# Performance work log

Hardware: AMD Instinct MI355X
Metric: run time of the kernel (lower is better)

## Reference

```python
import jax, jax.numpy as jnp
import numpy as np

N = 50000      # nodes (cells)
E = 800000     # directed edges
IN, H1, H2, Z = 512, 128, 128, 64


def setup_inputs() -> dict:
    key = jax.random.key(0)
    ks = jax.random.split(key, 12)
    x = jax.random.normal(ks[0], (N, IN), jnp.float32)
    edge_index = jax.random.randint(ks[1], (2, E), 0, N, dtype=jnp.int64)

    def glorot(k, i, o):
        return jax.random.normal(k, (i, o), jnp.float32) * np.float32(1.0 / np.sqrt(i))

    return {
        "x": x,
        "edge_index": edge_index,
        "W1": glorot(ks[2], IN, H1), "b1": jnp.zeros((H1,), jnp.float32),
        "W2": glorot(ks[3], H1, H2), "b2": jnp.zeros((H2,), jnp.float32),
        "Wm": glorot(ks[4], H2, Z),  "bm": jnp.zeros((Z,), jnp.float32),
        "Ws": glorot(ks[5], H2, Z),  "bs": jnp.zeros((Z,), jnp.float32),
    }


def _gcn_norm(edge_index, n):
    # PyG GCNConv default: add self-loops, sym-normalize D^-1/2 (A+I) D^-1/2
    loops = jnp.arange(n, dtype=edge_index.dtype)
    src = jnp.concatenate([edge_index[0], loops])
    dst = jnp.concatenate([edge_index[1], loops])
    deg = jax.ops.segment_sum(jnp.ones_like(dst, jnp.float32), dst, num_segments=n)
    dis = jnp.where(deg > 0, jax.lax.rsqrt(jnp.maximum(deg, 1.0)), 0.0)
    norm = dis[src] * dis[dst]  # [E+N]
    return src, dst, norm


def _gcn_conv(x, W, b, src, dst, norm, n):
    h = x @ W                          # [N, out] transform first
    msg = h[src] * norm[:, None]       # gather + scale
    out = jax.ops.segment_sum(msg, dst, num_segments=n)  # scatter-add at targets
    return out + b


def reference(x, edge_index, W1, b1, W2, b2, Wm, bm, Ws, bs):
    n = x.shape[0]
    src, dst, norm = _gcn_norm(edge_index, n)
    h = jax.nn.relu(_gcn_conv(x, W1, b1, src, dst, norm, n))
    h = jax.nn.relu(_gcn_conv(h, W2, b2, src, dst, norm, n))
    # dropout p=0.4 is identity in eval mode
    z_mean = _gcn_conv(h, Wm, bm, src, dst, norm, n)
    z_log_std = _gcn_conv(h, Ws, bs, src, dst, norm, n)
    return (z_mean, z_log_std)
```

## Files before the change

### kernel.cpp

```cpp
#include <hip/hip_runtime.h>


using u16 = unsigned short;
typedef __attribute__((ext_vector_type(8))) short short8;
typedef __attribute__((ext_vector_type(4))) float f32x4;

__device__ __forceinline__ void split_bf16(float f, u16& hi, u16& lo) {
    unsigned b = __float_as_uint(f);
    hi = (u16)(b >> 16);
    float rem = f - __uint_as_float(b & 0xFFFF0000u);
    lo = (u16)(__float_as_uint(rem) >> 16);
}

__device__ __forceinline__ int block_mode(const int* __restrict__ ew, int* sflag) {
    if (threadIdx.x == 0) *sflag = 0;
    __syncthreads();
    if (ew[2 * (int)threadIdx.x + 1] != 0) atomicOr(sflag, 1);
    __syncthreads();
    return *sflag ? 0 : 1;
}

__global__ void deg_kernel(const int* __restrict__ ew, int* __restrict__ deg, int E) {
    __shared__ int sflag;
    int mode = block_mode(ew, &sflag);
    int e = blockIdx.x * blockDim.x + threadIdx.x;
    if (e >= E) return;
    int d = mode ? ew[2 * E + 2 * e] : ew[E + e];
    atomicAdd(&deg[d], 1);
}

__global__ void scan_block_kernel(const int* __restrict__ deg, int* __restrict__ rowptr,
                                  int* __restrict__ aux, float* __restrict__ dis, int N) {
    __shared__ int s[256];
    int i = blockIdx.x * 256 + threadIdx.x;
    int v = (i < N) ? deg[i] : 0;
    if (i < N) dis[i] = rsqrtf((float)v + 1.0f);
    s[threadIdx.x] = v;
    __syncthreads();
    for (int off = 1; off < 256; off <<= 1) {
        int t = (threadIdx.x >= off) ? s[threadIdx.x - off] : 0;
        __syncthreads();
        s[threadIdx.x] += t;
        __syncthreads();
    }
    if (i < N) rowptr[i] = s[threadIdx.x] - v;
    if (threadIdx.x == 255) aux[blockIdx.x] = s[255];
}

__global__ void scan_aux_kernel(int* __restrict__ aux, int nb) {
    __shared__ int s[256];
    int i = threadIdx.x;
    int v = (i < nb) ? aux[i] : 0;
    s[i] = v;
    __syncthreads();
    for (int off = 1; off < 256; off <<= 1) {
        int t = (i >= off) ? s[i - off] : 0;
        __syncthreads();
        s[i] += t;
        __syncthreads();
    }
    if (i < nb) aux[i] = s[i] - v;
}

__global__ void add_offsets_kernel(int* __restrict__ rowptr, const int* __restrict__ aux,
                                   int N, int E) {
    int i = blockIdx.x * 256 + threadIdx.x;
    if (i < N) rowptr[i] += aux[i >> 8];
    if (i == 0) rowptr[N] = E;
}

__global__ void fill_csr_kernel(const int* __restrict__ ew,
                                const int* __restrict__ rowptr, int* __restrict__ cursor,
                                int* __restrict__ csr_src, int E) {
    __shared__ int sflag;
    int mode = block_mode(ew, &sflag);
    int e = blockIdx.x * blockDim.x + threadIdx.x;
    if (e >= E) return;
    int s = mode ? ew[2 * e] : ew[e];
    int d = mode ? ew[2 * E + 2 * e] : ew[E + e];
    int pos = rowptr[d] + atomicAdd(&cursor[d], 1);
    csr_src[pos] = s;
}

__global__ void conv_all_kernel(const float* __restrict__ W1, const float* __restrict__ W2,
                                const float* __restrict__ Wm, const float* __restrict__ Ws,
                                u16* __restrict__ W1t_hi, u16* __restrict__ W1t_lo,
                                u16* __restrict__ W2t_hi, u16* __restrict__ W2t_lo,
                                u16* __restrict__ Wct_hi, u16* __restrict__ Wct_lo) {
    int idx = blockIdx.x * 256 + threadIdx.x;
    u16 h, l;
    if (idx < 65536) {
        int k = idx >> 7, n = idx & 127;
        split_bf16(W1[idx], h, l);
        W1t_hi[n * 512 + k] = h;
        W1t_lo[n * 512 + k] = l;
    } else if (idx < 81920) {
        int t = idx - 65536;
        int k = t >> 7, n = t & 127;
        split_bf16(W2[t], h, l);
        W2t_hi[n * 128 + k] = h;
        W2t_lo[n * 128 + k] = l;
    } else if (idx < 98304) {
        int t = idx - 81920;
        int k = t >> 7, j = t & 127;
        float f = (j < 64) ? Wm[k * 64 + j] : Ws[k * 64 + (j - 64)];
        split_bf16(f, h, l);
        Wct_hi[j * 128 + k] = h;
        Wct_lo[j * 128 + k] = l;
    }
}

__global__ __launch_bounds__(256) void gemm_mfma(const float* __restrict__ A,
                                                 const u16* __restrict__ Bt_hi,
                                                 const u16* __restrict__ Bt_lo,
                                                 float* __restrict__ C,
                                                 int N, int K) {
    const int tid = threadIdx.x;
    const int w = tid >> 6, lane = tid & 63;
    const int m16 = lane & 15, quad = lane >> 4;

    const int nrt = (N + 31) >> 5;
    const int wtile = blockIdx.x * 4 + w;
    if (wtile >= 2 * nrt) return;
    const int rt = wtile >> 1;
    const int c0 = (wtile & 1) << 6;
    const int row0 = rt << 5;

    int r0 = row0 + m16;      if (r0 > N - 1) r0 = N - 1;
    int r1 = row0 + 16 + m16; if (r1 > N - 1) r1 = N - 1;
    const float* ap0 = A + (size_t)r0 * K + quad * 8;
    const float* ap1 = A + (size_t)r1 * K + quad * 8;
    const u16* bph = Bt_hi + (size_t)(c0 + m16) * K + quad * 8;
    const u16* bpl = Bt_lo + (size_t)(c0 + m16) * K + quad * 8;
    const size_t bstr = (size_t)16 * K;

    f32x4 acc[2][4];
#pragma unroll
    for (int i = 0; i < 2; ++i)
#pragma unroll
        for (int j = 0; j < 4; ++j) acc[i][j] = (f32x4)0.f;

    f32x4 x0, x1, x2, x3;
    f32x4 y0, y1, y2, y3;

    auto lda = [&](f32x4& v0, f32x4& v1, f32x4& v2, f32x4& v3, int kk) {
        const float* p0 = ap0 + kk * 32;
        const float* p1 = ap1 + kk * 32;
        v0 = *(const f32x4*)p0;
        v1 = *(const f32x4*)(p0 + 4);
        v2 = *(const f32x4*)p1;
        v3 = *(const f32x4*)(p1 + 4);
    };
    auto cvt = [&](const f32x4& v0, const f32x4& v1, short8& h, short8& l) {
#pragma unroll
        for (int q = 0; q < 4; ++q) {
            u16 hh, ll;
            split_bf16(v0[q], hh, ll);
            h[q] = (short)hh;
            l[q] = (short)ll;
            split_bf16(v1[q], hh, ll);
            h[4 + q] = (short)hh;
            l[4 + q] = (short)ll;
        }
    };
    auto step = [&](f32x4& v0, f32x4& v1, f32x4& v2, f32x4& v3,
                    int kk, int kpre, bool pre) {
        short8 bh[4], bl[4];
#pragma unroll
        for (int j = 0; j < 4; ++j) {
            bh[j] = *(const short8*)(bph + bstr * j + kk * 32);
            bl[j] = *(const short8*)(bpl + bstr * j + kk * 32);
        }
        short8 ah[2], al[2];
        cvt(v0, v1, ah[0], al[0]);
        cvt(v2, v3, ah[1], al[1]);
        if (pre) lda(v0, v1, v2, v3, kpre);
#pragma unroll
        for (int i = 0; i < 2; ++i)
#pragma unroll
            for (int j = 0; j < 4; ++j) {
                acc[i][j] = __builtin_amdgcn_mfma_f32_16x16x32_bf16(
                    ah[i], bh[j], acc[i][j], 0, 0, 0);
                acc[i][j] = __builtin_amdgcn_mfma_f32_16x16x32_bf16(
                    ah[i], bl[j], acc[i][j], 0, 0, 0);
                acc[i][j] = __builtin_amdgcn_mfma_f32_16x16x32_bf16(
                    al[i], bh[j], acc[i][j], 0, 0, 0);
            }
    };

    const int ksteps = K >> 5;
    lda(x0, x1, x2, x3, 0);
    lda(y0, y1, y2, y3, 1);
    int ks = 0;
    for (; ks + 2 < ksteps; ks += 2) {
        step(x0, x1, x2, x3, ks, ks + 2, true);
        step(y0, y1, y2, y3, ks + 1, ks + 3, true);
    }
    step(x0, x1, x2, x3, ks, 0, false);
    step(y0, y1, y2, y3, ks + 1, 0, false);

#pragma unroll
    for (int i = 0; i < 2; ++i) {
#pragma unroll
        for (int r = 0; r < 4; ++r) {
            int gr = row0 + i * 16 + quad * 4 + r;
            if (gr < N) {
#pragma unroll
                for (int j = 0; j < 4; ++j)
                    C[(size_t)gr * 128 + c0 + j * 16 + m16] = acc[i][j][r];
            }
        }
    }
}

__global__ __launch_bounds__(256) void propagate_kernel(
    const float* __restrict__ h, const int* __restrict__ rowptr,
    const int* __restrict__ csr_src, const float* __restrict__ dis,
    const float* __restrict__ bias, float* __restrict__ out, int N, int do_relu) {
    int wave = (blockIdx.x * 256 + threadIdx.x) >> 6;
    int lane = threadIdx.x & 63;
    if (wave >= N) return;
    int v = wave;
    int f = lane * 2;
    float dv = dis[v];
    float ax = 0.f, ay = 0.f;
    int beg = rowptr[v], end = rowptr[v + 1];
    int i = beg;
    for (; i + 8 <= end; i += 8) {
        int s[8];
        float ww[8];
        float2 g[8];
#pragma unroll
        for (int u = 0; u < 8; ++u) s[u] = csr_src[i + u];
#pragma unroll
        for (int u = 0; u < 8; ++u) ww[u] = dis[s[u]];
#pragma unroll
        for (int u = 0; u < 8; ++u) g[u] = *(const float2*)&h[(size_t)s[u] * 128 + f];
#pragma unroll
        for (int u = 0; u < 8; ++u) {
            float t = ww[u] * dv;
            ax += t * g[u].x;
            ay += t * g[u].y;
        }
    }
    if (i + 4 <= end) {
        int s[4];
        float ww[4];
        float2 g[4];
#pragma unroll
        for (int u = 0; u < 4; ++u) s[u] = csr_src[i + u];
#pragma unroll
        for (int u = 0; u < 4; ++u) ww[u] = dis[s[u]];
#pragma unroll
        for (int u = 0; u < 4; ++u) g[u] = *(const float2*)&h[(size_t)s[u] * 128 + f];
#pragma unroll
        for (int u = 0; u < 4; ++u) {
            float t = ww[u] * dv;
            ax += t * g[u].x;
            ay += t * g[u].y;
        }
        i += 4;
    }
    for (; i < end; ++i) {
        int s = csr_src[i];
        float ws = dis[s] * dv;
        float2 g = *(const float2*)&h[(size_t)s * 128 + f];
        ax += ws * g.x;
        ay += ws * g.y;
    }
    float2 hv = *(const float2*)&h[(size_t)v * 128 + f];
    ax += dv * dv * hv.x;
    ay += dv * dv * hv.y;
    ax += bias[f];
    ay += bias[f + 1];
    if (do_relu) { ax = fmaxf(ax, 0.f); ay = fmaxf(ay, 0.f); }
    *(float2*)&out[(size_t)v * 128 + f] = make_float2(ax, ay);
}

__global__ __launch_bounds__(256) void propagate_final_kernel(
    const float* __restrict__ h, const int* __restrict__ rowptr,
    const int* __restrict__ csr_src, const float* __restrict__ dis,
    const float* __restrict__ bm, const float* __restrict__ bs,
    float* __restrict__ out, int N) {
    int wave = (blockIdx.x * 256 + threadIdx.x) >> 6;
    int lane = threadIdx.x & 63;
    if (wave >= N) return;
    int v = wave;
    int f = lane * 2;
    float dv = dis[v];
    float ax = 0.f, ay = 0.f;
    int beg = rowptr[v], end = rowptr[v + 1];
    int i = beg;
    for (; i + 8 <= end; i += 8) {
        int s[8];
        float ww[8];
        float2 g[8];
#pragma unroll
        for (int u = 0; u < 8; ++u) s[u] = csr_src[i + u];
#pragma unroll
        for (int u = 0; u < 8; ++u) ww[u] = dis[s[u]];
#pragma unroll
        for (int u = 0; u < 8; ++u) g[u] = *(const float2*)&h[(size_t)s[u] * 128 + f];
#pragma unroll
        for (int u = 0; u < 8; ++u) {
            float t = ww[u] * dv;
            ax += t * g[u].x;
            ay += t * g[u].y;
        }
    }
    if (i + 4 <= end) {
        int s[4];
        float ww[4];
        float2 g[4];
#pragma unroll
        for (int u = 0; u < 4; ++u) s[u] = csr_src[i + u];
#pragma unroll
        for (int u = 0; u < 4; ++u) ww[u] = dis[s[u]];
#pragma unroll
        for (int u = 0; u < 4; ++u) g[u] = *(const float2*)&h[(size_t)s[u] * 128 + f];
#pragma unroll
        for (int u = 0; u < 4; ++u) {
            float t = ww[u] * dv;
            ax += t * g[u].x;
            ay += t * g[u].y;
        }
        i += 4;
    }
    for (; i < end; ++i) {
        int s = csr_src[i];
        float ws = dis[s] * dv;
        float2 g = *(const float2*)&h[(size_t)s * 128 + f];
        ax += ws * g.x;
        ay += ws * g.y;
    }
    float2 hv = *(const float2*)&h[(size_t)v * 128 + f];
    ax += dv * dv * hv.x;
    ay += dv * dv * hv.y;
    if (f < 64) {
        *(float2*)&out[(size_t)v * 64 + f] = make_float2(ax + bm[f], ay + bm[f + 1]);
    } else {
        int g = f - 64;
        *(float2*)&out[(size_t)N * 64 + (size_t)v * 64 + g] =
            make_float2(ax + bs[g], ay + bs[g + 1]);
    }
}

extern "C" void kernel_launch(void* const* d_in, const int* in_sizes, int n_in,
                              void* d_out, int out_size, void* d_ws, size_t ws_size,
                              hipStream_t stream) {
    const float* x  = (const float*)d_in[0];
    const int*   ew = (const int*)d_in[1];
    const float* W1 = (const float*)d_in[2];
    const float* b1 = (const float*)d_in[3];
    const float* W2 = (const float*)d_in[4];
    const float* b2 = (const float*)d_in[5];
    const float* Wm = (const float*)d_in[6];
    const float* bm = (const float*)d_in[7];
    const float* Ws = (const float*)d_in[8];
    const float* bs = (const float*)d_in[9];
    float* out = (float*)d_out;

    const int IN = 512, H = 128;
    const int N = in_sizes[0] / IN;
    const int E = in_sizes[1] / 2;

    char* base = (char*)d_ws;
    size_t off = 0;
    auto alloc = [&](size_t bytes) -> char* {
        char* p = base + off;
        off = (off + bytes + 255) & ~(size_t)255;
        return p;
    };
    char*  degcur  = (char*) alloc(400384);
    float* dis     = (float*)alloc((size_t)N * 4);
    int*   rowptr  = (int*)  alloc((size_t)(N + 1) * 4);
    int*   aux     = (int*)  alloc(256 * 4);
    int*   csr_src = (int*)  alloc((size_t)E * 4);
    u16*   W1t_hi  = (u16*)  alloc((size_t)IN * H * 2);
    u16*   W1t_lo  = (u16*)  alloc((size_t)IN * H * 2);
    u16*   W2t_hi  = (u16*)  alloc((size_t)H * H * 2);
    u16*   W2t_lo  = (u16*)  alloc((size_t)H * H * 2);
    u16*   Wct_hi  = (u16*)  alloc((size_t)H * H * 2);
    u16*   Wct_lo  = (u16*)  alloc((size_t)H * H * 2);
    float* hA      = (float*)alloc((size_t)N * H * 4);
    float* hB      = (float*)alloc((size_t)N * H * 4);
    (void)ws_size; (void)n_in; (void)out_size;

    int* deg    = (int*)degcur;
    int* cursor = (int*)(degcur + 200192);

    hipMemsetAsync(degcur, 0, 400384, stream);

    const int eblocks = (E + 255) / 256;
    const int nblocks = (N + 255) / 256;

    conv_all_kernel<<<(98304 + 255) / 256, 256, 0, stream>>>(
        W1, W2, Wm, Ws, W1t_hi, W1t_lo, W2t_hi, W2t_lo, Wct_hi, Wct_lo);
    deg_kernel<<<eblocks, 256, 0, stream>>>(ew, deg, E);
    scan_block_kernel<<<nblocks, 256, 0, stream>>>(deg, rowptr, aux, dis, N);
    scan_aux_kernel<<<1, 256, 0, stream>>>(aux, nblocks);
    add_offsets_kernel<<<nblocks, 256, 0, stream>>>(rowptr, aux, N, E);
    fill_csr_kernel<<<eblocks, 256, 0, stream>>>(ew, rowptr, cursor, csr_src, E);

    const int wtiles = 2 * ((N + 31) / 32);
    const int gblocks = (wtiles + 3) / 4;
    const int pblocks = (N * 64 + 255) / 256;

    gemm_mfma<<<gblocks, 256, 0, stream>>>(x, W1t_hi, W1t_lo, hA, N, IN);
    propagate_kernel<<<pblocks, 256, 0, stream>>>(hA, rowptr, csr_src, dis,
                                                  b1, hB, N, 1);
    gemm_mfma<<<gblocks, 256, 0, stream>>>(hB, W2t_hi, W2t_lo, hA, N, H);
    propagate_kernel<<<pblocks, 256, 0, stream>>>(hA, rowptr, csr_src, dis,
                                                  b2, hB, N, 1);
    gemm_mfma<<<gblocks, 256, 0, stream>>>(hB, Wct_hi, Wct_lo, hA, N, H);
    propagate_final_kernel<<<pblocks, 256, 0, stream>>>(hA, rowptr, csr_src, dis,
                                                        bm, bs, out, N);
}
```

Before: 551.3 us.

## Stage GEMM B tiles in double-buffered shared memory shared across waves

The GEMM block now covers a 64x128 output tile, with four waves that share the B (weight) fragments staged cooperatively through double-buffered LDS, padded to avoid bank conflicts. Previously each wave loaded its B fragments directly from global memory. The change is meant to cut redundant global and L2 traffic for the weights. In exchange it adds a __syncthreads per K step and LDS pressure. Since the weights are small and already cache-resident, the gain may be limited, and the whole pipeline is dominated by the propagate kernels.

```diff
diff --git a/kernel.cpp b/kernel.cpp
--- a/kernel.cpp
+++ b/kernel.cpp
@@ -110,29 +110,36 @@
     }
 }
 
+#define TILE_OFF(t) ((t) * 520)
+
 __global__ __launch_bounds__(256) void gemm_mfma(const float* __restrict__ A,
                                                  const u16* __restrict__ Bt_hi,
                                                  const u16* __restrict__ Bt_lo,
                                                  float* __restrict__ C,
                                                  int N, int K) {
+    __shared__ __align__(16) u16 BsH[2][8 * 520], BsL[2][8 * 520];
+
     const int tid = threadIdx.x;
     const int w = tid >> 6, lane = tid & 63;
     const int m16 = lane & 15, quad = lane >> 4;
 
-    const int nrt = (N + 31) >> 5;
-    const int wtile = blockIdx.x * 4 + w;
-    if (wtile >= 2 * nrt) return;
-    const int rt = wtile >> 1;
-    const int c0 = (wtile & 1) << 6;
-    const int row0 = rt << 5;
-
-    int r0 = row0 + m16;      if (r0 > N - 1) r0 = N - 1;
-    int r1 = row0 + 16 + m16; if (r1 > N - 1) r1 = N - 1;
+    const int row0 = blockIdx.x * 64;
+    const int R = (w >> 1) * 32;
+    const int c0 = (w & 1) << 6;
+    const int btile = (w & 1) * 4;
+
+    const int s_bc = tid >> 1;
+    const int s_bk = (tid & 1) * 16;
+    const int b_q0 = (tid & 1) * 2;
+    const int b_dst0 = TILE_OFF(s_bc >> 4) + ((s_bc & 15) + 16 * (b_q0 + 0)) * 8;
+    const int b_dst1 = TILE_OFF(s_bc >> 4) + ((s_bc & 15) + 16 * (b_q0 + 1)) * 8;
+    const u16* bph = Bt_hi + (size_t)s_bc * K + s_bk;
+    const u16* bpl = Bt_lo + (size_t)s_bc * K + s_bk;
+
+    int r0 = row0 + R + m16;      if (r0 > N - 1) r0 = N - 1;
+    int r1 = row0 + R + 16 + m16; if (r1 > N - 1) r1 = N - 1;
     const float* ap0 = A + (size_t)r0 * K + quad * 8;
     const float* ap1 = A + (size_t)r1 * K + quad * 8;
-    const u16* bph = Bt_hi + (size_t)(c0 + m16) * K + quad * 8;
-    const u16* bpl = Bt_lo + (size_t)(c0 + m16) * K + quad * 8;
-    const size_t bstr = (size_t)16 * K;
 
     f32x4 acc[2][4];
 #pragma unroll
@@ -142,7 +149,20 @@
 
     f32x4 x0, x1, x2, x3;
     f32x4 y0, y1, y2, y3;
-
+    short8 rbh0, rbh1, rbl0, rbl1;
+
+    auto ldb = [&](int kk) {
+        rbh0 = *(const short8*)(bph + kk * 32);
+        rbh1 = *(const short8*)(bph + kk * 32 + 8);
+        rbl0 = *(const short8*)(bpl + kk * 32);
+        rbl1 = *(const short8*)(bpl + kk * 32 + 8);
+    };
+    auto stb = [&](int buf) {
+        *(short8*)&BsH[buf][b_dst0] = rbh0;
+        *(short8*)&BsH[buf][b_dst1] = rbh1;
+        *(short8*)&BsL[buf][b_dst0] = rbl0;
+        *(short8*)&BsL[buf][b_dst1] = rbl1;
+    };
     auto lda = [&](f32x4& v0, f32x4& v1, f32x4& v2, f32x4& v3, int kk) {
         const float* p0 = ap0 + kk * 32;
         const float* p1 = ap1 + kk * 32;
@@ -163,47 +183,56 @@
             l[4 + q] = (short)ll;
         }
     };
-    auto step = [&](f32x4& v0, f32x4& v1, f32x4& v2, f32x4& v3,
-                    int kk, int kpre, bool pre) {
-        short8 bh[4], bl[4];
+
+    const int ksteps = K >> 5;
+    ldb(0);
+    lda(x0, x1, x2, x3, 0);
+    lda(y0, y1, y2, y3, 1);
+    stb(0);
+    ldb(1);
+
+    for (int ks = 0; ks < ksteps; ++ks) {
+        const int buf = ks & 1;
+        __syncthreads();
+        if (ks + 1 < ksteps) stb(buf ^ 1);
+        if (ks + 2 < ksteps) ldb(ks + 2);
+
+        short8 fbh[4], fbl[4];
 #pragma unroll
         for (int j = 0; j < 4; ++j) {
-            bh[j] = *(const short8*)(bph + bstr * j + kk * 32);
-            bl[j] = *(const short8*)(bpl + bstr * j + kk * 32);
-        }
+            fbh[j] = *(const short8*)&BsH[buf][TILE_OFF(btile + j) + lane * 8];
+            fbl[j] = *(const short8*)&BsL[buf][TILE_OFF(btile + j) + lane * 8];
+        }
+
         short8 ah[2], al[2];
-        cvt(v0, v1, ah[0], al[0]);
-        cvt(v2, v3, ah[1], al[1]);
-        if (pre) lda(v0, v1, v2, v3, kpre);
+        if (buf) {
+            cvt(y0, y1, ah[0], al[0]);
+            cvt(y2, y3, ah[1], al[1]);
+            if (ks + 2 < ksteps) lda(y0, y1, y2, y3, ks + 2);
+        } else {
+            cvt(x0, x1, ah[0], al[0]);
+            cvt(x2, x3, ah[1], al[1]);
+            if (ks + 2 < ksteps) lda(x0, x1, x2, x3, ks + 2);
+        }
+
 #pragma unroll
         for (int i = 0; i < 2; ++i)
 #pragma unroll
             for (int j = 0; j < 4; ++j) {
                 acc[i][j] = __builtin_amdgcn_mfma_f32_16x16x32_bf16(
-                    ah[i], bh[j], acc[i][j], 0, 0, 0);
+                    ah[i], fbh[j], acc[i][j], 0, 0, 0);
                 acc[i][j] = __builtin_amdgcn_mfma_f32_16x16x32_bf16(
-                    ah[i], bl[j], acc[i][j], 0, 0, 0);
+                    ah[i], fbl[j], acc[i][j], 0, 0, 0);
                 acc[i][j] = __builtin_amdgcn_mfma_f32_16x16x32_bf16(
-                    al[i], bh[j], acc[i][j], 0, 0, 0);
+                    al[i], fbh[j], acc[i][j], 0, 0, 0);
             }
-    };
-
-    const int ksteps = K >> 5;
-    lda(x0, x1, x2, x3, 0);
-    lda(y0, y1, y2, y3, 1);
-    int ks = 0;
-    for (; ks + 2 < ksteps; ks += 2) {
-        step(x0, x1, x2, x3, ks, ks + 2, true);
-        step(y0, y1, y2, y3, ks + 1, ks + 3, true);
-    }
-    step(x0, x1, x2, x3, ks, 0, false);
-    step(y0, y1, y2, y3, ks + 1, 0, false);
+    }
 
 #pragma unroll
     for (int i = 0; i < 2; ++i) {
 #pragma unroll
         for (int r = 0; r < 4; ++r) {
-            int gr = row0 + i * 16 + quad * 4 + r;
+            int gr = row0 + R + i * 16 + quad * 4 + r;
             if (gr < N) {
 #pragma unroll
                 for (int j = 0; j < 4; ++j)
@@ -277,7 +306,7 @@
     *(float2*)&out[(size_t)v * 128 + f] = make_float2(ax, ay);
 }
 
-__global__ __launch_bounds__(256) void propagate_final_kernel(
+__global__ void __launch_bounds__(256) propagate_final_kernel(
     const float* __restrict__ h, const int* __restrict__ rowptr,
     const int* __restrict__ csr_src, const float* __restrict__ dis,
     const float* __restrict__ bm, const float* __restrict__ bs,
@@ -402,8 +431,7 @@
     add_offsets_kernel<<<nblocks, 256, 0, stream>>>(rowptr, aux, N, E);
     fill_csr_kernel<<<eblocks, 256, 0, stream>>>(ew, rowptr, cursor, csr_src, E);
 
-    const int wtiles = 2 * ((N + 31) / 32);
-    const int gblocks = (wtiles + 3) / 4;
+    const int gblocks = (N + 63) / 64;
     const int pblocks = (N * 64 + 255) / 256;
 
     gemm_mfma<<<gblocks, 256, 0, stream>>>(x, W1t_hi, W1t_lo, hA, N, IN);
```

Measured after the change: 522.0 us. 1.06x faster.
